# Optimization experiments

Measured on AMD Instinct MI355X. Metric: run time of the kernel, lower is better.

Reference implementation:

```python
import jax, jax.numpy as jnp
import numpy as np
from jax import lax

K = 5  # nearest neighbors (includes self)
EPS = 1e-6


def _relu(a):
    return jnp.maximum(a, 0.0)


def setup_inputs() -> dict:
    key = jax.random.key(0)
    ks = jax.random.split(key, 16)
    B, N, D = 8, 4096, 2
    LD = 64  # local_dim

    def w(k, fan_in, fan_out):
        return jax.random.normal(k, (fan_in, fan_out), jnp.float32) / np.sqrt(fan_in)

    x = jax.random.normal(ks[0], (B, N, D), jnp.float32)
    inp = {
        "x": x,
        # local_mlp: D->64->128->LD
        "lw1": w(ks[1], D, 64), "lb1": jnp.zeros((64,), jnp.float32),
        "lw2": w(ks[2], 64, 128), "lb2": jnp.zeros((128,), jnp.float32),
        "lw3": w(ks[3], 128, LD), "lb3": jnp.zeros((LD,), jnp.float32),
        # cls_branch: (D+LD)->128->128
        "cw1": w(ks[4], D + LD, 128), "cb1": jnp.zeros((128,), jnp.float32),
        "cw2": w(ks[5], 128, 128), "cb2": jnp.zeros((128,), jnp.float32),
        # topo_branch: LD->128->128
        "tw1": w(ks[6], LD, 128), "tb1": jnp.zeros((128,), jnp.float32),
        "tw2": w(ks[7], 128, 128), "tb2": jnp.zeros((128,), jnp.float32),
    }
    return inp


def reference(x, lw1, lb1, lw2, lb2, lw3, lb3,
              cw1, cb1, cw2, cb2, tw1, tb1, tw2, tb2):
    B, N, D = x.shape
    # squared pairwise distances (B,N,N)
    sq = jnp.sum(x * x, axis=-1)
    dist_sq = sq[:, :, None] + sq[:, None, :] - 2.0 * jnp.einsum("bnd,bmd->bnm", x, x)
    _, idx = lax.top_k(-dist_sq, K)  # (B,N,K) nearest (self first)

    neighbors = x[jnp.arange(B)[:, None, None], idx]          # (B,N,K,D)
    rel = neighbors - x[:, :, None, :]                         # relative coords
    centered = rel - rel.mean(axis=2, keepdims=True)           # (B,N,K,D)
    cov = jnp.einsum("bnki,bnkj->bnij", centered, centered) / (K - 1)

    e, v = jnp.linalg.eigh(cov + EPS * jnp.eye(2, dtype=x.dtype))  # ascending eigvals
    v1 = v[..., :, 1]                                          # principal eigenvector
    base_angle = jnp.arctan2(v1[..., 1], v1[..., 0])[..., None]  # (B,N,1)

    base_axes = jnp.sqrt(jnp.maximum(e, EPS))                  # (B,N,2)
    base_axes = base_axes[..., ::-1]                           # descending: major first
    base_axes = base_axes / (base_axes.max(axis=-1, keepdims=True) + EPS)
    base_axes = jnp.maximum(base_axes, 0.2)

    lcc = jnp.einsum("bnki,bnij->bnkj", centered, v)           # canonical coords
    h = _relu(lcc @ lw1 + lb1)
    h = _relu(h @ lw2 + lb2)
    h = _relu(h @ lw3 + lb3)                                   # (B,N,K,LD)
    local_feats = h.max(axis=2)                                # (B,N,LD)

    cls_in = jnp.concatenate([x, local_feats], axis=-1)
    cls_features = _relu(_relu(cls_in @ cw1 + cb1) @ cw2 + cb2)
    topo_features = _relu(_relu(local_feats @ tw1 + tb1) @ tw2 + tb2)
    return (cls_features, topo_features, base_angle, base_axes)
```

## Files before the change

kernel.cpp:

```cpp
#include <hip/hip_runtime.h>
#include <math.h>

#pragma clang fp contract(off)

#define NPTS 4096
#define PTS  32768
#define ROWS 163840
#define SLOTS 8

#define GRID  32
#define NCELL (GRID * GRID)
#define GL    5.0f
#define GSC   3.2f
#define CW    0.3125f

#define EPS_L   5.9604644775390625e-8f
#define EPS2_L  3.5527136788005009e-15f
#define SAFMIN_L 1.1754943508222875e-38f

__device__ __forceinline__ float frn_mul(float a, float b) { float r = a * b; return r; }
__device__ __forceinline__ float frn_add(float a, float b) { float r = a + b; return r; }
__device__ __forceinline__ float frn_sub(float a, float b) { float r = a - b; return r; }
__device__ __forceinline__ float frn_div(float a, float b) { float r = a / b; return r; }

__device__ __forceinline__ float ref_sq(float x0, float x1) {
  return frn_add(frn_mul(x0, x0), frn_mul(x1, x1));
}
__device__ __forceinline__ float ref_key(float nx, float ny, float sqn,
                                         float mx, float my, float sqm) {
  float dot = fmaf(ny, my, frn_mul(nx, mx));
  float s = frn_add(sqn, sqm);
  return fmaf(-2.0f, dot, s);
}

__device__ __forceinline__ int cell_of(float v) {
  int c = (int)floorf((v + GL) * GSC);
  return min(max(c, 0), GRID - 1);
}

__global__ __launch_bounds__(256) void prep_w(
    const float* __restrict__ lw1, const float* __restrict__ lw2, const float* __restrict__ lw3,
    const float* __restrict__ cw1, const float* __restrict__ cw2,
    const float* __restrict__ tw1, const float* __restrict__ tw2,
    float* __restrict__ wt) {
  const int Ks[7]   = {2, 64, 128, 66, 128, 64, 128};
  const int Kp[7]   = {2, 64, 128, 80, 128, 64, 128};
  const int Ns[7]   = {64, 128, 64, 128, 128, 128, 128};
  const int offs[7] = {0, 128, 8320, 16512, 26752, 43136, 51328};
  const float* srcs[7] = {lw1, lw2, lw3, cw1, cw2, tw1, tw2};
  int b = blockIdx.x;
  const float* src = srcs[b];
  float* dst = wt + offs[b];
  int K = Ks[b], KP = Kp[b], N = Ns[b];
  for (int e = threadIdx.x; e < KP * N; e += 256) {
    int j = e / KP, i = e - j * KP;
    dst[e] = (i < K) ? src[i * N + j] : 0.0f;
  }
}

__global__ __launch_bounds__(128) void grid_hist(const float* __restrict__ x,
                                                 unsigned int* __restrict__ hist) {
  int p = blockIdx.x * 128 + threadIdx.x;
  float2 me = ((const float2*)x)[p];
  int b = p >> 12;
  int cx = cell_of(me.x), cy = cell_of(me.y);
  atomicAdd(&hist[b * NCELL + cy * GRID + cx], 1u);
}

__global__ __launch_bounds__(1024) void grid_scan(const unsigned int* __restrict__ hist,
                                                  unsigned int* __restrict__ base,
                                                  unsigned int* __restrict__ cursor) {
  __shared__ unsigned int sh[NCELL];
  int b = blockIdx.x, t = threadIdx.x;
  unsigned int v = hist[b * NCELL + t];
  sh[t] = v;
  __syncthreads();
  for (int off = 1; off < NCELL; off <<= 1) {
    unsigned int u = (t >= off) ? sh[t - off] : 0u;
    __syncthreads();
    sh[t] += u;
    __syncthreads();
  }
  unsigned int g = (unsigned int)(b * NPTS) + sh[t] - v;
  base[b * NCELL + t] = g;
  cursor[b * NCELL + t] = g;
}

__global__ __launch_bounds__(128) void grid_scatter(const float* __restrict__ x,
                                                    unsigned int* __restrict__ cursor,
                                                    float2* __restrict__ sxy,
                                                    unsigned int* __restrict__ sid) {
  int p = blockIdx.x * 128 + threadIdx.x;
  float2 me = ((const float2*)x)[p];
  int b = p >> 12;
  int cx = cell_of(me.x), cy = cell_of(me.y);
  unsigned int slot = atomicAdd(&cursor[b * NCELL + cy * GRID + cx], 1u);
  sxy[slot] = me;
  sid[slot] = (unsigned int)(p & (NPTS - 1));
}

#define VISIT_CELL(cx, cy) do {                                        \
    int _cell = (cy) * GRID + (cx);                                    \
    unsigned int _st = cb[_cell];                                      \
    unsigned int _en = _st + ch[_cell];                                \
    for (unsigned int _i = _st; _i < _en; _i++) {                      \
      float2 _c = sxy[_i];                                             \
      unsigned int _ci = sid[_i];                                      \
      float _dx = me.x - _c.x, _dy = me.y - _c.y;                      \
      float _dist = fmaf(_dy, _dy, _dx * _dx);                         \
      unsigned int _v = (__float_as_uint(_dist) & 0xFFFFF000u) | _ci;  \
      _Pragma("unroll")                                                \
      for (int _k = 0; _k < SLOTS; _k++) {                             \
        unsigned int _lo = min(_v, d[_k]);                             \
        unsigned int _hi = max(_v, d[_k]);                             \
        d[_k] = _lo; _v = _hi;                                         \
      }                                                                \
    }                                                                  \
  } while (0)

__global__ __launch_bounds__(128) void grid_query(
    const float2* __restrict__ sxy, const unsigned int* __restrict__ sid,
    const unsigned int* __restrict__ base, const unsigned int* __restrict__ hist,
    unsigned int* __restrict__ ipart) {
  int s = blockIdx.x * 128 + threadIdx.x;
  int b = s >> 12;
  float2 me = sxy[s];
  int myloc = (int)sid[s];
  int hx = cell_of(me.x), hy = cell_of(me.y);
  const unsigned int* cb = base + b * NCELL;
  const unsigned int* ch = hist + b * NCELL;
  unsigned int d[SLOTS];
#pragma unroll
  for (int k = 0; k < SLOTS; k++) d[k] = 0xFFFFFFFFu;
  for (int r = 0; r < GRID; r++) {
    if (r >= 2) {
      float lb = (float)(r - 1) * CW;
      float lbsq = lb * lb * 0.999f;
      unsigned int vb = __float_as_uint(lbsq) & 0xFFFFF000u;
      if (vb > d[SLOTS - 1]) break;
    }
    int x0 = max(hx - r, 0), x1 = min(hx + r, GRID - 1);
    int y0 = max(hy - r, 0), y1 = min(hy + r, GRID - 1);
    for (int cy = y0; cy <= y1; cy++) {
      if (cy == hy - r || cy == hy + r) {
        for (int cx = x0; cx <= x1; cx++) VISIT_CELL(cx, cy);
      } else {
        if (hx - r >= 0)        VISIT_CELL(hx - r, cy);
        if (hx + r <= GRID - 1) VISIT_CELL(hx + r, cy);
      }
    }
  }
  int gp = b * NPTS + myloc;
#pragma unroll
  for (int k = 0; k < SLOTS; k++) ipart[(size_t)k * PTS + gp] = d[k];
}

__global__ __launch_bounds__(128) void merge_geom(const float* __restrict__ x,
    const unsigned int* __restrict__ ipart,
    float2* __restrict__ lcct2,
    float* __restrict__ angle_out, float2* __restrict__ axes_out,
    float* __restrict__ lftx) {
  int p = blockIdx.x * 128 + threadIdx.x;
  int batch = p >> 12;
  const float2* xb = (const float2*)(x + (size_t)batch * NPTS * 2);
  float2 me = ((const float2*)x)[p];
  lftx[p] = me.x;
  lftx[PTS + p] = me.y;
#pragma unroll
  for (int r = 66; r < 80; r++) lftx[(size_t)r * PTS + p] = 0.0f;
  float sqn = ref_sq(me.x, me.y);

  unsigned int g[SLOTS];
#pragma unroll
  for (int s = 0; s < SLOTS; s++) g[s] = ipart[(size_t)s * PTS + p];

  float dk[5]; int id[5];
#pragma unroll
  for (int s = 0; s < 5; s++) { dk[s] = 3.0e38f; id[s] = 0x7fffffff; }
#pragma unroll
  for (int s8 = 0; s8 < SLOTS; s8++) {
    int ci = (int)(g[s8] & 0xFFFu);
    float2 c = xb[ci];
    float key = ref_key(me.x, me.y, sqn, c.x, c.y, ref_sq(c.x, c.y));
    float v = key; int vi = ci;
#pragma unroll
    for (int s = 0; s < 5; s++) {
      bool lt = (v < dk[s]) || (v == dk[s] && vi < id[s]);
      float tv = dk[s]; int ti = id[s];
      if (lt) { dk[s] = v; id[s] = vi; v = tv; vi = ti; }
    }
  }
  float rx[5], ry[5];
  float sx = 0.f, sy = 0.f;
#pragma unroll
  for (int k = 0; k < 5; k++) {
    float2 nb = xb[id[k]];
    rx[k] = frn_sub(nb.x, me.x); ry[k] = frn_sub(nb.y, me.y);
    sx = frn_add(sx, rx[k]); sy = frn_add(sy, ry[k]);
  }
  float mx = frn_div(sx, 5.0f), my = frn_div(sy, 5.0f);
  float c00 = 0.f, c01 = 0.f, c11 = 0.f;
#pragma unroll
  for (int k = 0; k < 5; k++) {
    rx[k] = frn_sub(rx[k], mx); ry[k] = frn_sub(ry[k], my);
    c00 = frn_add(c00, frn_mul(rx[k], rx[k]));
    c01 = frn_add(c01, frn_mul(rx[k], ry[k]));
    c11 = frn_add(c11, frn_mul(ry[k], ry[k]));
  }
  c00 = frn_div(c00, 4.0f); c01 = frn_div(c01, 4.0f); c11 = frn_div(c11, 4.0f);
  float A = frn_add(c00, 1e-6f), Bv = c01, C = frn_add(c11, 1e-6f);

  float absA = fabsf(A), absC = fabsf(C), absB = fabsf(Bv);
  float thr = frn_mul(frn_mul(sqrtf(absA), sqrtf(absC)), EPS_L);
  bool diag = (absB == 0.f) || (absB <= thr);
  if (!diag) {
    bool qr = (absC < absA);
    float b2 = frn_mul(absB, absB);
    float t = qr ? frn_add(frn_mul(frn_mul(EPS2_L, absC), absA), SAFMIN_L)
                 : frn_add(frn_mul(frn_mul(EPS2_L, absA), absC), SAFMIN_L);
    if (b2 <= t) diag = true;
  }
  float e1, e2, v00, v10, v01, v11;
  if (diag) {
    if (C < A) { e1 = C; e2 = A; v00 = 0.f; v10 = 1.f; v01 = 1.f; v11 = 0.f; }
    else       { e1 = A; e2 = C; v00 = 1.f; v10 = 0.f; v01 = 0.f; v11 = 1.f; }
  } else {
    float sm = frn_add(A, C), df = frn_sub(A, C);
    float adf = fabsf(df), tb = frn_add(Bv, Bv), ab = fabsf(tb);
    float rt;
    if (adf > ab) {
      float r = frn_div(ab, adf);
      rt = frn_mul(adf, sqrtf(frn_add(1.0f, frn_mul(r, r))));
    } else if (adf < ab) {
      float r = frn_div(adf, ab);
      rt = frn_mul(ab, sqrtf(frn_add(1.0f, frn_mul(r, r))));
    } else {
      rt = frn_mul(ab, sqrtf(2.0f));
    }
    float acmx, acmn;
    if (absA > absC) { acmx = A; acmn = C; } else { acmx = C; acmn = A; }
    float rt1, rt2; int sgn1;
    if (sm < 0.f) {
      rt1 = frn_mul(0.5f, frn_sub(sm, rt)); sgn1 = -1;
      rt2 = frn_sub(frn_mul(frn_div(acmx, rt1), acmn), frn_mul(frn_div(Bv, rt1), Bv));
    } else if (sm > 0.f) {
      rt1 = frn_mul(0.5f, frn_add(sm, rt)); sgn1 = 1;
      rt2 = frn_sub(frn_mul(frn_div(acmx, rt1), acmn), frn_mul(frn_div(Bv, rt1), Bv));
    } else {
      rt1 = frn_mul(0.5f, rt); rt2 = frn_mul(-0.5f, rt); sgn1 = 1;
    }
    float cs, cs1, sn1; int sgn2;
    if (df >= 0.f) { cs = frn_add(df, rt); sgn2 = 1; }
    else           { cs = frn_sub(df, rt); sgn2 = -1; }
    float acs = fabsf(cs);
    if (acs > ab) {
      float ct = frn_div(-tb, cs);
      sn1 = frn_div(1.0f, sqrtf(frn_add(1.0f, frn_mul(ct, ct))));
      cs1 = frn_mul(ct, sn1);
    } else {
      if (ab == 0.f) { cs1 = 1.0f; sn1 = 0.0f; }
      else {
        float tn = frn_div(-cs, tb);
        cs1 = frn_div(1.0f, sqrtf(frn_add(1.0f, frn_mul(tn, tn))));
        sn1 = frn_mul(tn, cs1);
      }
    }
    if (sgn1 == sgn2) { float t = cs1; cs1 = -sn1; sn1 = t; }
    if (rt2 < rt1) { e1 = rt2; e2 = rt1; v00 = -sn1; v10 = cs1; v01 = cs1;  v11 = sn1; }
    else           { e1 = rt1; e2 = rt2; v00 = cs1;  v10 = sn1; v01 = -sn1; v11 = cs1; }
  }

  angle_out[p] = atan2f(v11, v01);
  float aM = sqrtf(fmaxf(e2, 1e-6f));
  float am = sqrtf(fmaxf(e1, 1e-6f));
  float den = frn_add(fmaxf(aM, am), 1e-6f);
  axes_out[p] = make_float2(fmaxf(frn_div(aM, den), 0.2f),
                            fmaxf(frn_div(am, den), 0.2f));

  size_t rowb = (size_t)p * 5;
#pragma unroll
  for (int k = 0; k < 5; k++) {
    float l0 = frn_add(frn_mul(rx[k], v00), frn_mul(ry[k], v10));
    float l1 = frn_add(frn_mul(rx[k], v01), frn_mul(ry[k], v11));
    lcct2[rowb + k] = make_float2(l0, l1);
  }
}

__global__ __launch_bounds__(256, 3) void gemm_l2(
    const float2* __restrict__ lcct2, const float* __restrict__ lw1t,
    const float* __restrict__ lb1,
    const float* __restrict__ wt, const float* __restrict__ bias,
    float* __restrict__ out_t, int M) {
  __shared__ float alds[16 * 128];
  __shared__ float wlds[16 * 128];
  __shared__ float w1s[192];
  int t = threadIdx.x;
  int m0 = blockIdx.x * 128;
  if (t < 192) w1s[t] = (t < 128) ? lw1t[t] : lb1[t - 128];
  int mloc = t & 127;
  int kbase = t >> 7;
  float2 lme = lcct2[m0 + mloc];
  int tm = t & 15;
  int tn = t >> 4;
  float acc[8][8];
#pragma unroll
  for (int j = 0; j < 8; j++) {
    float b = bias[tn * 8 + j];
#pragma unroll
    for (int i = 0; i < 8; i++) acc[j][i] = b;
  }
  for (int kt = 0; kt < 4; kt++) {
    int k0 = kt * 16;
    __syncthreads();
#pragma unroll
    for (int pp = 0; pp < 8; pp++) {
      int kk = pp * 2 + kbase;
      int k = k0 + kk;
      float h = fmaf(lme.y, w1s[2 * k + 1], fmaf(lme.x, w1s[2 * k], w1s[128 + k]));
      alds[kk * 128 + mloc] = fmaxf(h, 0.f);
    }
#pragma unroll
    for (int pp = 0; pp < 2; pp++) {
      int e = pp * 256 + t;
      int n = e >> 2;
      int kc = e & 3;
      float4 v = *(const float4*)(wt + (size_t)n * 64 + k0 + kc * 4);
      wlds[(kc * 4 + 0) * 128 + n] = v.x;
      wlds[(kc * 4 + 1) * 128 + n] = v.y;
      wlds[(kc * 4 + 2) * 128 + n] = v.z;
      wlds[(kc * 4 + 3) * 128 + n] = v.w;
    }
    __syncthreads();
#pragma unroll
    for (int kk = 0; kk < 16; kk++) {
      float af[8], wf[8];
      *(float4*)(af)     = *(const float4*)(alds + kk * 128 + tm * 8);
      *(float4*)(af + 4) = *(const float4*)(alds + kk * 128 + tm * 8 + 4);
      *(float4*)(wf)     = *(const float4*)(wlds + kk * 128 + tn * 8);
      *(float4*)(wf + 4) = *(const float4*)(wlds + kk * 128 + tn * 8 + 4);
#pragma unroll
      for (int j = 0; j < 8; j++)
#pragma unroll
        for (int i = 0; i < 8; i++)
          acc[j][i] = fmaf(af[i], wf[j], acc[j][i]);
    }
  }
#pragma unroll
  for (int j = 0; j < 8; j++) {
    int n = tn * 8 + j;
    float4 o0, o1;
    o0.x = fmaxf(acc[j][0], 0.f); o0.y = fmaxf(acc[j][1], 0.f);
    o0.z = fmaxf(acc[j][2], 0.f); o0.w = fmaxf(acc[j][3], 0.f);
    o1.x = fmaxf(acc[j][4], 0.f); o1.y = fmaxf(acc[j][5], 0.f);
    o1.z = fmaxf(acc[j][6], 0.f); o1.w = fmaxf(acc[j][7], 0.f);
    float* dst = out_t + (size_t)n * M + m0 + tm * 8;
    *(float4*)(dst) = o0;
    *(float4*)(dst + 4) = o1;
  }
}

__global__ __launch_bounds__(512, 4) void gemm_l3max(
    const float* __restrict__ h2, const float* __restrict__ wt,
    const float* __restrict__ bias, float* __restrict__ lftx) {
  __shared__ float alds[16 * 320];
  __shared__ float wlds[16 * 64];
  int t = threadIdx.x;
  int m0 = blockIdx.x * 320;
  int pt = t & 63;
  int ng = t >> 6;
  float acc[5][8];
#pragma unroll
  for (int j = 0; j < 8; j++) {
    float b = bias[ng * 8 + j];
#pragma unroll
    for (int r = 0; r < 5; r++) acc[r][j] = b;
  }
  for (int kt = 0; kt < 8; kt++) {
    int k0 = kt * 16;
    __syncthreads();
    for (int e = t; e < 1280; e += 512) {
      int kk = e / 80;
      int m4 = e - kk * 80;
      float4 v = *(const float4*)(h2 + (size_t)(k0 + kk) * ROWS + m0 + m4 * 4);
      *(float4*)(alds + kk * 320 + m4 * 4) = v;
    }
    if (t < 256) {
      int n = t >> 2, kc = t & 3;
      float4 v = *(const float4*)(wt + (size_t)n * 128 + k0 + kc * 4);
      wlds[(kc * 4 + 0) * 64 + n] = v.x;
      wlds[(kc * 4 + 1) * 64 + n] = v.y;
      wlds[(kc * 4 + 2) * 64 + n] = v.z;
      wlds[(kc * 4 + 3) * 64 + n] = v.w;
    }
    __syncthreads();
#pragma unroll
    for (int kk = 0; kk < 16; kk++) {
      float af[5], wf[8];
#pragma unroll
      for (int r = 0; r < 5; r++) af[r] = alds[kk * 320 + pt * 5 + r];
      *(float4*)(wf)     = *(const float4*)(wlds + kk * 64 + ng * 8);
      *(float4*)(wf + 4) = *(const float4*)(wlds + kk * 64 + ng * 8 + 4);
#pragma unroll
      for (int r = 0; r < 5; r++)
#pragma unroll
        for (int j = 0; j < 8; j++)
          acc[r][j] = fmaf(af[r], wf[j], acc[r][j]);
    }
  }
  int p = blockIdx.x * 64 + pt;
#pragma unroll
  for (int j = 0; j < 8; j++) {
    float r0 = fmaxf(acc[0][j], 0.f), r1 = fmaxf(acc[1][j], 0.f);
    float r2 = fmaxf(acc[2][j], 0.f), r3 = fmaxf(acc[3][j], 0.f);
    float r4 = fmaxf(acc[4][j], 0.f);
    float m = fmaxf(fmaxf(fmaxf(r0, r1), fmaxf(r2, r3)), r4);
    lftx[(size_t)(ng * 8 + j + 2) * PTS + p] = m;
  }
}

__global__ __launch_bounds__(256, 3) void gemm_head1(
    const float* __restrict__ lftx, const float* __restrict__ wtbase,
    const float* __restrict__ cb1, const float* __restrict__ tb1,
    float* __restrict__ a1c, float* __restrict__ a1t) {
  __shared__ float alds[16 * 128];
  __shared__ float wlds[16 * 128];
  int bid = blockIdx.x;
  bool isC = bid < 256;
  const float* in_t = isC ? lftx : (lftx + 2 * PTS);
  const float* wt   = isC ? (wtbase + 16512) : (wtbase + 43136);
  const float* bias = isC ? cb1 : tb1;
  float* out_t      = isC ? a1c : a1t;
  int Kstr = isC ? 80 : 64;
  int KT   = isC ? 5 : 4;
  int m0 = (bid & 255) * 128;
  int t = threadIdx.x;
  int tm = t & 15;
  int tn = t >> 4;
  float acc[8][8];
#pragma unroll
  for (int j = 0; j < 8; j++) {
    float b = bias[tn * 8 + j];
#pragma unroll
    for (int i = 0; i < 8; i++) acc[j][i] = b;
  }
  for (int kt = 0; kt < KT; kt++) {
    int k0 = kt * 16;
    __syncthreads();
#pragma unroll
    for (int pp = 0; pp < 2; pp++) {
      int e = pp * 256 + t;
      int kk = e >> 5;
      int m4 = e & 31;
      float4 v = *(const float4*)(in_t + (size_t)(k0 + kk) * PTS + m0 + m4 * 4);
      *(float4*)(alds + kk * 128 + m4 * 4) = v;
    }
#pragma unroll
    for (int pp = 0; pp < 2; pp++) {
      int e = pp * 256 + t;
      int n = e >> 2;
      int kc = e & 3;
      float4 v = *(const float4*)(wt + (size_t)n * Kstr + k0 + kc * 4);
      wlds[(kc * 4 + 0) * 128 + n] = v.x;
      wlds[(kc * 4 + 1) * 128 + n] = v.y;
      wlds[(kc * 4 + 2) * 128 + n] = v.z;
      wlds[(kc * 4 + 3) * 128 + n] = v.w;
    }
    __syncthreads();
#pragma unroll
    for (int kk = 0; kk < 16; kk++) {
      float af[8], wf[8];
      *(float4*)(af)     = *(const float4*)(alds + kk * 128 + tm * 8);
      *(float4*)(af + 4) = *(const float4*)(alds + kk * 128 + tm * 8 + 4);
      *(float4*)(wf)     = *(const float4*)(wlds + kk * 128 + tn * 8);
      *(float4*)(wf + 4) = *(const float4*)(wlds + kk * 128 + tn * 8 + 4);
#pragma unroll
      for (int j = 0; j < 8; j++)
#pragma unroll
        for (int i = 0; i < 8; i++)
          acc[j][i] = fmaf(af[i], wf[j], acc[j][i]);
    }
  }
#pragma unroll
  for (int j = 0; j < 8; j++) {
    int n = tn * 8 + j;
    float4 o0, o1;
    o0.x = fmaxf(acc[j][0], 0.f); o0.y = fmaxf(acc[j][1], 0.f);
    o0.z = fmaxf(acc[j][2], 0.f); o0.w = fmaxf(acc[j][3], 0.f);
    o1.x = fmaxf(acc[j][4], 0.f); o1.y = fmaxf(acc[j][5], 0.f);
    o1.z = fmaxf(acc[j][6], 0.f); o1.w = fmaxf(acc[j][7], 0.f);
    float* dst = out_t + (size_t)n * PTS + m0 + tm * 8;
    *(float4*)(dst) = o0;
    *(float4*)(dst + 4) = o1;
  }
}

__global__ __launch_bounds__(256, 3) void gemm_head2(
    const float* __restrict__ a1c, const float* __restrict__ a1t,
    const float* __restrict__ wtbase,
    const float* __restrict__ cb2, const float* __restrict__ tb2,
    float* __restrict__ outbase) {
  __shared__ float alds[16 * 128];
  __shared__ float wlds[16 * 128];
  int bid = blockIdx.x;
  bool isC = bid < 256;
  const float* in_t = isC ? a1c : a1t;
  const float* wt   = isC ? (wtbase + 26752) : (wtbase + 51328);
  const float* bias = isC ? cb2 : tb2;
  float* out        = isC ? outbase : (outbase + 4194304);
  int m0 = (bid & 255) * 128;
  int t = threadIdx.x;
  int tm = t & 15;
  int tn = t >> 4;
  float acc[8][8];
#pragma unroll
  for (int j = 0; j < 8; j++) {
    float b = bias[tn * 8 + j];
#pragma unroll
    for (int i = 0; i < 8; i++) acc[j][i] = b;
  }
  for (int kt = 0; kt < 8; kt++) {
    int k0 = kt * 16;
    __syncthreads();
#pragma unroll
    for (int pp = 0; pp < 2; pp++) {
      int e = pp * 256 + t;
      int kk = e >> 5;
      int m4 = e & 31;
      float4 v = *(const float4*)(in_t + (size_t)(k0 + kk) * PTS + m0 + m4 * 4);
      *(float4*)(alds + kk * 128 + m4 * 4) = v;
    }
#pragma unroll
    for (int pp = 0; pp < 2; pp++) {
      int e = pp * 256 + t;
      int n = e >> 2;
      int kc = e & 3;
      float4 v = *(const float4*)(wt + (size_t)n * 128 + k0 + kc * 4);
      wlds[(kc * 4 + 0) * 128 + n] = v.x;
      wlds[(kc * 4 + 1) * 128 + n] = v.y;
      wlds[(kc * 4 + 2) * 128 + n] = v.z;
      wlds[(kc * 4 + 3) * 128 + n] = v.w;
    }
    __syncthreads();
#pragma unroll
    for (int kk = 0; kk < 16; kk++) {
      float af[8], wf[8];
      *(float4*)(af)     = *(const float4*)(alds + kk * 128 + tm * 8);
      *(float4*)(af + 4) = *(const float4*)(alds + kk * 128 + tm * 8 + 4);
      *(float4*)(wf)     = *(const float4*)(wlds + kk * 128 + tn * 8);
      *(float4*)(wf + 4) = *(const float4*)(wlds + kk * 128 + tn * 8 + 4);
#pragma unroll
      for (int j = 0; j < 8; j++)
#pragma unroll
        for (int i = 0; i < 8; i++)
          acc[j][i] = fmaf(af[i], wf[j], acc[j][i]);
    }
  }
#pragma unroll
  for (int i = 0; i < 8; i++) {
    int m = m0 + tm * 8 + i;
    float4 o0, o1;
    o0.x = fmaxf(acc[0][i], 0.f); o0.y = fmaxf(acc[1][i], 0.f);
    o0.z = fmaxf(acc[2][i], 0.f); o0.w = fmaxf(acc[3][i], 0.f);
    o1.x = fmaxf(acc[4][i], 0.f); o1.y = fmaxf(acc[5][i], 0.f);
    o1.z = fmaxf(acc[6][i], 0.f); o1.w = fmaxf(acc[7][i], 0.f);
    float* dst = out + (size_t)m * 128 + tn * 8;
    *(float4*)(dst) = o0;
    *(float4*)(dst + 4) = o1;
  }
}

extern "C" void kernel_launch(void* const* d_in, const int* in_sizes, int n_in,
                              void* d_out, int out_size, void* d_ws, size_t ws_size,
                              hipStream_t stream) {
  const float* x   = (const float*)d_in[0];
  const float* lb1 = (const float*)d_in[2];
  const float* lb2 = (const float*)d_in[4];
  const float* lb3 = (const float*)d_in[6];
  const float* cb1 = (const float*)d_in[8];
  const float* cb2 = (const float*)d_in[10];
  const float* tb1 = (const float*)d_in[12];
  const float* tb2 = (const float*)d_in[14];

  float* out = (float*)d_out;
  float* angle_out = out + 8388608;
  float* axes_out  = out + 8421376;

  float* W = (float*)d_ws;
  float* wt    = W;
  float* R1    = W + 67712;
  float* R2    = R1 + 10485760;
  float* R3    = R2 + 10485760;
  float* lftx  = R3 + 20971520;
  float* lcct2 = lftx + 2621440;
  float* gbuf  = lcct2 + 327680;
  unsigned int* ipart  = (unsigned int*)R1;
  float* a1c   = R2;
  float* a1t   = R2 + 4194304;
  float* h2    = R3;
  unsigned int* hist   = (unsigned int*)gbuf;
  unsigned int* gbase  = hist + 8 * NCELL;
  unsigned int* cursor = gbase + 8 * NCELL;
  unsigned int* sid    = cursor + 8 * NCELL;
  float2* sxy          = (float2*)(sid + PTS);

  prep_w<<<7, 256, 0, stream>>>((const float*)d_in[1], (const float*)d_in[3], (const float*)d_in[5],
                                (const float*)d_in[7], (const float*)d_in[9],
                                (const float*)d_in[11], (const float*)d_in[13], wt);
  hipMemsetAsync(hist, 0, 8 * NCELL * sizeof(unsigned int), stream);
  grid_hist<<<PTS / 128, 128, 0, stream>>>(x, hist);
  grid_scan<<<8, NCELL, 0, stream>>>(hist, gbase, cursor);
  grid_scatter<<<PTS / 128, 128, 0, stream>>>(x, cursor, sxy, sid);
  grid_query<<<PTS / 128, 128, 0, stream>>>(sxy, sid, gbase, hist, ipart);
  merge_geom<<<256, 128, 0, stream>>>(x, ipart, (float2*)lcct2, angle_out, (float2*)axes_out, lftx);

  gemm_l2<<<ROWS / 128, 256, 0, stream>>>((const float2*)lcct2, wt + 0, lb1,
                                          wt + 128, lb2, h2, ROWS);
  gemm_l3max<<<PTS / 64, 512, 0, stream>>>(h2, wt + 8320, lb3, lftx);

  gemm_head1<<<512, 256, 0, stream>>>(lftx, wt, cb1, tb1, a1c, a1t);
  gemm_head2<<<512, 256, 0, stream>>>(a1c, a1t, wt, cb2, tb2, out);
}
```

Before: 351.3 us.

## Split kNN grid query across four lanes per point with shuffle merge

```diff
diff --git a/kernel.cpp b/kernel.cpp
--- a/kernel.cpp
+++ b/kernel.cpp
@@ -88,27 +88,25 @@
 
 __global__ __launch_bounds__(128) void grid_scatter(const float* __restrict__ x,
                                                     unsigned int* __restrict__ cursor,
-                                                    float2* __restrict__ sxy,
-                                                    unsigned int* __restrict__ sid) {
+                                                    float4* __restrict__ scand) {
   int p = blockIdx.x * 128 + threadIdx.x;
   float2 me = ((const float2*)x)[p];
   int b = p >> 12;
   int cx = cell_of(me.x), cy = cell_of(me.y);
   unsigned int slot = atomicAdd(&cursor[b * NCELL + cy * GRID + cx], 1u);
-  sxy[slot] = me;
-  sid[slot] = (unsigned int)(p & (NPTS - 1));
+  scand[slot] = make_float4(me.x, me.y, __uint_as_float((unsigned int)(p & (NPTS - 1))), 0.f);
 }
 
 #define VISIT_CELL(cx, cy) do {                                        \
     int _cell = (cy) * GRID + (cx);                                    \
     unsigned int _st = cb[_cell];                                      \
     unsigned int _en = _st + ch[_cell];                                \
-    for (unsigned int _i = _st; _i < _en; _i++) {                      \
-      float2 _c = sxy[_i];                                             \
-      unsigned int _ci = sid[_i];                                      \
+    for (unsigned int _i = _st + sub; _i < _en; _i += 4) {             \
+      float4 _c = scand[_i];                                           \
       float _dx = me.x - _c.x, _dy = me.y - _c.y;                      \
       float _dist = fmaf(_dy, _dy, _dx * _dx);                         \
-      unsigned int _v = (__float_as_uint(_dist) & 0xFFFFF000u) | _ci;  \
+      unsigned int _v = (__float_as_uint(_dist) & 0xFFFFF000u)         \
+                        | __float_as_uint(_c.z);                       \
       _Pragma("unroll")                                                \
       for (int _k = 0; _k < SLOTS; _k++) {                             \
         unsigned int _lo = min(_v, d[_k]);                             \
@@ -118,14 +116,19 @@
     }                                                                  \
   } while (0)
 
-__global__ __launch_bounds__(128) void grid_query(
-    const float2* __restrict__ sxy, const unsigned int* __restrict__ sid,
+#define CAS(a, b) { unsigned int _l = min(a, b), _h = max(a, b); a = _l; b = _h; }
+
+__global__ __launch_bounds__(256) void grid_query(
+    const float4* __restrict__ scand,
     const unsigned int* __restrict__ base, const unsigned int* __restrict__ hist,
     unsigned int* __restrict__ ipart) {
-  int s = blockIdx.x * 128 + threadIdx.x;
+  int tid = blockIdx.x * 256 + threadIdx.x;
+  int s = tid >> 2;
+  unsigned int sub = tid & 3;
   int b = s >> 12;
-  float2 me = sxy[s];
-  int myloc = (int)sid[s];
+  float4 mec = scand[s];
+  float2 me = make_float2(mec.x, mec.y);
+  int myloc = (int)__float_as_uint(mec.z);
   int hx = cell_of(me.x), hy = cell_of(me.y);
   const unsigned int* cb = base + b * NCELL;
   const unsigned int* ch = hist + b * NCELL;
@@ -150,9 +153,26 @@
       }
     }
   }
-  int gp = b * NPTS + myloc;
-#pragma unroll
-  for (int k = 0; k < SLOTS; k++) ipart[(size_t)k * PTS + gp] = d[k];
+#pragma unroll
+  for (int m = 1; m <= 2; m <<= 1) {
+    unsigned int pd[SLOTS];
+#pragma unroll
+    for (int k = 0; k < SLOTS; k++)
+      pd[k] = (unsigned int)__shfl_xor((int)d[k], m);
+    unsigned int t[SLOTS];
+#pragma unroll
+    for (int k = 0; k < SLOTS; k++) t[k] = min(d[k], pd[SLOTS - 1 - k]);
+    CAS(t[0], t[4]); CAS(t[1], t[5]); CAS(t[2], t[6]); CAS(t[3], t[7]);
+    CAS(t[0], t[2]); CAS(t[1], t[3]); CAS(t[4], t[6]); CAS(t[5], t[7]);
+    CAS(t[0], t[1]); CAS(t[2], t[3]); CAS(t[4], t[5]); CAS(t[6], t[7]);
+#pragma unroll
+    for (int k = 0; k < SLOTS; k++) d[k] = t[k];
+  }
+  if (sub == 0) {
+    int gp = b * NPTS + myloc;
+#pragma unroll
+    for (int k = 0; k < SLOTS; k++) ipart[(size_t)k * PTS + gp] = d[k];
+  }
 }
 
 __global__ __launch_bounds__(128) void merge_geom(const float* __restrict__ x,
@@ -600,8 +620,7 @@
   unsigned int* hist   = (unsigned int*)gbuf;
   unsigned int* gbase  = hist + 8 * NCELL;
   unsigned int* cursor = gbase + 8 * NCELL;
-  unsigned int* sid    = cursor + 8 * NCELL;
-  float2* sxy          = (float2*)(sid + PTS);
+  float4* scand        = (float4*)(cursor + 8 * NCELL);
 
   prep_w<<<7, 256, 0, stream>>>((const float*)d_in[1], (const float*)d_in[3], (const float*)d_in[5],
                                 (const float*)d_in[7], (const float*)d_in[9],
@@ -609,8 +628,8 @@
   hipMemsetAsync(hist, 0, 8 * NCELL * sizeof(unsigned int), stream);
   grid_hist<<<PTS / 128, 128, 0, stream>>>(x, hist);
   grid_scan<<<8, NCELL, 0, stream>>>(hist, gbase, cursor);
-  grid_scatter<<<PTS / 128, 128, 0, stream>>>(x, cursor, sxy, sid);
-  grid_query<<<PTS / 128, 128, 0, stream>>>(sxy, sid, gbase, hist, ipart);
+  grid_scatter<<<PTS / 128, 128, 0, stream>>>(x, cursor, scand);
+  grid_query<<<(PTS * 4) / 256, 256, 0, stream>>>(scand, gbase, hist, ipart);
   merge_geom<<<256, 128, 0, stream>>>(x, ipart, (float2*)lcct2, angle_out, (float2*)axes_out, lftx);
 
   gemm_l2<<<ROWS / 128, 256, 0, stream>>>((const float2*)lcct2, wt + 0, lb1,
```

New measurement: 385.8 us. 1.1x slower.
